# Kernel optimization log

Hardware: AMD Instinct MI355X
Metric: run time of the kernel (lower is better)

## Reference

```python
import jax, jax.numpy as jnp
import numpy as np
from jax import lax

N_QUANTIZE = 256
N_AUX = 28
N_RESCH = 512
N_SKIPCH = 256
KS = 2
DILATIONS = [2 ** i for i in range(10)] * 3  # 30 layers
L = len(DILATIONS)


def _causal_conv(x, w, b, d):
    # x: (B, Cin, T), w: (Cout, Cin, KS) torch Conv1d layout, left-pad => causal
    pad = (w.shape[-1] - 1) * d
    y = lax.conv_general_dilated(x, w, window_strides=(1,), padding=[(pad, 0)],
                                 rhs_dilation=(d,),
                                 dimension_numbers=('NCH', 'OIH', 'NCH'))
    return y + b[None, :, None]


def _conv1x1(x, w, b):
    # x: (B, Cin, T), w: (Cout, Cin)
    return jnp.einsum('oi,bit->bot', w, x) + b[None, :, None]


def setup_inputs() -> dict:
    key = jax.random.key(0)
    ks = jax.random.split(key, 20)
    B, T = 2, 8000
    s = 0.05
    rn = lambda k, shape: (jax.random.normal(k, shape, jnp.float32) * s)
    inp = {
        'x': jax.random.randint(ks[0], (B, T), 0, N_QUANTIZE),
        'h': jax.random.normal(ks[1], (B, N_AUX, T), jnp.float32),
        'causal_w': rn(ks[2], (N_RESCH, N_QUANTIZE, KS)),
        'causal_b': rn(ks[3], (N_RESCH,)),
        'dil_sig_w': rn(ks[4], (L, N_RESCH, N_RESCH, KS)),
        'dil_sig_b': rn(ks[5], (L, N_RESCH)),
        'dil_tanh_w': rn(ks[6], (L, N_RESCH, N_RESCH, KS)),
        'dil_tanh_b': rn(ks[7], (L, N_RESCH)),
        'aux_sig_w': rn(ks[8], (L, N_RESCH, N_AUX)),
        'aux_sig_b': rn(ks[9], (L, N_RESCH)),
        'aux_tanh_w': rn(ks[10], (L, N_RESCH, N_AUX)),
        'aux_tanh_b': rn(ks[11], (L, N_RESCH)),
        'skip_w': rn(ks[12], (L, N_SKIPCH, N_RESCH)),
        'skip_b': rn(ks[13], (L, N_SKIPCH)),
        'res_w': rn(ks[14], (L, N_RESCH, N_RESCH)),
        'res_b': rn(ks[15], (L, N_RESCH)),
        'post1_w': rn(ks[16], (N_SKIPCH, N_SKIPCH)),
        'post1_b': rn(ks[17], (N_SKIPCH,)),
        'post2_w': rn(ks[18], (N_QUANTIZE, N_SKIPCH)),
        'post2_b': rn(ks[19], (N_QUANTIZE,)),
    }
    return inp


def reference(x, h, causal_w, causal_b, dil_sig_w, dil_sig_b, dil_tanh_w, dil_tanh_b,
              aux_sig_w, aux_sig_b, aux_tanh_w, aux_tanh_b, skip_w, skip_b,
              res_w, res_b, post1_w, post1_b, post2_w, post2_b):
    B, T = x.shape
    # _preprocess: onehot (B,T,Q) -> (B,Q,T), then causal conv
    oh = jax.nn.one_hot(x % N_QUANTIZE, N_QUANTIZE, dtype=jnp.float32).transpose(0, 2, 1)
    out = _causal_conv(oh, causal_w, causal_b, 1)  # (B, n_resch, T)
    skip_sum = jnp.zeros((B, N_SKIPCH, T), jnp.float32)
    for l, d in enumerate(DILATIONS):
        sig = _causal_conv(out, dil_sig_w[l], dil_sig_b[l], d) + _conv1x1(h, aux_sig_w[l], aux_sig_b[l])
        tan = _causal_conv(out, dil_tanh_w[l], dil_tanh_b[l], d) + _conv1x1(h, aux_tanh_w[l], aux_tanh_b[l])
        z = jax.nn.sigmoid(sig) * jnp.tanh(tan)
        skip_sum = skip_sum + _conv1x1(z, skip_w[l], skip_b[l])
        out = _conv1x1(z, res_w[l], res_b[l]) + out
    # _postprocess: relu -> 1x1 -> relu -> 1x1 -> (B, T, n_quantize)
    y = jax.nn.relu(skip_sum)
    y = jax.nn.relu(_conv1x1(y, post1_w, post1_b))
    y = _conv1x1(y, post2_w, post2_b)
    return y.transpose(0, 2, 1)
```

## Files before the change

### kernel.cpp

```cpp
#include <hip/hip_runtime.h>
#include <math.h>

#define T_LEN 8000
#define BATCH 2
#define CCH 512
#define SKP 256
#define AUXP 32
#define NQ 256
#define NLAYER 30
#define PADF 512
#define TPAD 8192
#define ROWS (PADF + TPAD)
#define HROWS TPAD

typedef unsigned short hfu;
typedef unsigned int u32;
typedef __attribute__((ext_vector_type(8))) _Float16 half8;
typedef __attribute__((ext_vector_type(4))) float f32x4;

#define GLOAD16(g, l)                                                          \
  __builtin_amdgcn_global_load_lds(                                            \
      (const __attribute__((address_space(1))) void*)(g),                      \
      (__attribute__((address_space(3))) void*)(l), 16, 0, 0)

__device__ inline hfu hfbits(float f) {
  union { _Float16 h; hfu u; } x;
  x.h = (_Float16)f;
  return x.u;
}
__device__ inline u32 pk2(float a, float b) {
  return (u32)hfbits(a) | ((u32)hfbits(b) << 16);
}
__device__ inline uint4 pk8(const float f[8]) {
  return make_uint4(pk2(f[0], f[1]), pk2(f[2], f[3]), pk2(f[4], f[5]), pk2(f[6], f[7]));
}
__device__ inline int ldsL(int row, int ck) {
  return ((row >> 1) << 3) + ((((ck) ^ ((row >> 1) & 3)) << 1) | (row & 1));
}

__global__ __launch_bounds__(256) void zero16(uint4* p, int n) {
  for (int i = blockIdx.x * 256 + threadIdx.x; i < n; i += gridDim.x * 256)
    p[i] = make_uint4(0u, 0u, 0u, 0u);
}

__global__ __launch_bounds__(256) void cvt_dil2b(const float* __restrict__ inS,
                                                 const float* __restrict__ inT,
                                                 hfu* __restrict__ outS, hfu* __restrict__ outT) {
  const long NG = (long)NLAYER * CCH * (CCH / 8);
  for (long g2 = (long)blockIdx.x * 256 + threadIdx.x; g2 < 2 * NG; g2 += (long)gridDim.x * 256) {
    const int sel = (int)(g2 >= NG);
    const long g = sel ? (g2 - NG) : g2;
    const float* in = sel ? inT : inS;
    hfu* out = sel ? outT : outS;
    const int i8 = (int)(g & 63) * 8;
    const int o = (int)((g >> 6) & 511);
    const int l = (int)(g >> 15);
    const float* pp = in + (((size_t)l * CCH + o) * CCH + i8) * 2;
    float4 a = *(const float4*)pp;
    float4 bq = *(const float4*)(pp + 4);
    float4 c = *(const float4*)(pp + 8);
    float4 e = *(const float4*)(pp + 12);
    const float t0[8] = {a.x, a.z, bq.x, bq.z, c.x, c.z, e.x, e.z};
    const float t1[8] = {a.y, a.w, bq.y, bq.w, c.y, c.w, e.y, e.w};
    hfu* ob = out + ((size_t)l * 2 * CCH + o) * CCH + i8;
    *(uint4*)ob = pk8(t0);
    *(uint4*)(ob + (size_t)CCH * CCH) = pk8(t1);
  }
}

__global__ __launch_bounds__(256) void cvt_skipres(const float* __restrict__ skw,
                                                   const float* __restrict__ rsw,
                                                   hfu* __restrict__ out) {
  const long NG = (long)NLAYER * 768 * (CCH / 4);
  for (long g = (long)blockIdx.x * 256 + threadIdx.x; g < NG; g += (long)gridDim.x * 256) {
    const int i4 = (int)(g & 127) * 4;
    const int r = (int)((g >> 7) % 768);
    const int l = (int)(g / (128 * 768));
    const float* src = (r < SKP) ? (skw + ((size_t)l * SKP + r) * CCH + i4)
                                 : (rsw + ((size_t)l * CCH + (r - SKP)) * CCH + i4);
    float4 f = *(const float4*)src;
    *(uint2*)(out + ((size_t)l * 768 + r) * CCH + i4) = make_uint2(pk2(f.x, f.y), pk2(f.z, f.w));
  }
}

__global__ __launch_bounds__(256) void cvt_aux(const float* __restrict__ in, hfu* __restrict__ out) {
  const int N = NLAYER * CCH * AUXP;
  for (int i = blockIdx.x * 256 + threadIdx.x; i < N; i += gridDim.x * 256) {
    const int j = i & 31;
    const int o = (i >> 5) & 511;
    const int l = i >> 14;
    float v = (j < 28) ? in[((size_t)l * CCH + o) * 28 + j] : 0.f;
    out[i] = hfbits(v);
  }
}

__global__ __launch_bounds__(256) void cvt_copy(const float* __restrict__ in, hfu* __restrict__ out, int n) {
  for (int i = blockIdx.x * 256 + threadIdx.x; i < n; i += gridDim.x * 256)
    out[i] = hfbits(in[i]);
}

__global__ __launch_bounds__(256) void cvt_cwt(const float* __restrict__ cw, float* __restrict__ out) {
  const int N = 2 * NQ * CCH;
  for (int i = blockIdx.x * 256 + threadIdx.x; i < N; i += gridDim.x * 256) {
    const int tap = i >> 17;
    const int r = i & 131071;
    const int xq = r >> 9;
    const int o = r & 511;
    out[i] = cw[((size_t)o * NQ + xq) * 2 + tap];
  }
}

__global__ __launch_bounds__(256) void htrans_kernel(const float* __restrict__ h, hfu* __restrict__ hbf) {
  const int b = blockIdx.y;
  const int t = blockIdx.x * 64 + (threadIdx.x & 63);
  const int j0 = threadIdx.x >> 6;
#pragma unroll
  for (int j = j0; j < AUXP; j += 4) {
    float v = (j < 28 && t < T_LEN) ? h[((size_t)b * 28 + j) * T_LEN + t] : 0.f;
    hbf[((size_t)b * HROWS + t) * AUXP + j] = hfbits(v);
  }
}

template <int PRE>
__global__ __launch_bounds__(256) void embed_kernel(const int* __restrict__ x,
                                                    const float* __restrict__ cwt,
                                                    const float* __restrict__ cb,
                                                    float* __restrict__ outf,
                                                    hfu* __restrict__ outb) {
  const int b = blockIdx.y;
  const int t = blockIdx.x * 4 + (threadIdx.x >> 6);
  const int o = (threadIdx.x & 63) * 8;
  const int xc = x[(size_t)b * T_LEN + t] & 255;
  const int xp = (t > 0) ? (x[(size_t)b * T_LEN + t - 1] & 255) : 0;
  const float won = (t > 0) ? 1.f : 0.f;
  const float* c1 = cwt + 131072 + (size_t)xc * CCH + o;
  const float* c0 = cwt + (size_t)xp * CCH + o;
  float v[8];
#pragma unroll
  for (int j = 0; j < 8; ++j) v[j] = cb[o + j] + c1[j] + won * c0[j];
  if (PRE) {
    *(uint4*)&outb[((size_t)b * ROWS + PADF + t) * CCH + o] = pk8(v);
  } else {
    float* po = outf + ((size_t)b * ROWS + PADF + t) * CCH + o;
    *(float4*)po = make_float4(v[0], v[1], v[2], v[3]);
    *(float4*)(po + 4) = make_float4(v[4], v[5], v[6], v[7]);
  }
}

template <int PRE>
__global__ __launch_bounds__(512, 2) void gate_kernel(
    const hfu* __restrict__ actb, const float* __restrict__ actf,
    const hfu* __restrict__ hbf,
    const void* __restrict__ wsp, const void* __restrict__ wtp,
    const hfu* __restrict__ auxs, const hfu* __restrict__ auxt,
    const float* __restrict__ bs1, const float* __restrict__ bs2,
    const float* __restrict__ bt1, const float* __restrict__ bt2,
    hfu* __restrict__ z, int d) {
  extern __shared__ uint4 smd[];
  const int tid = threadIdx.x;
  const int lane = tid & 63, wid = tid >> 6;
  const int wm = wid >> 2, wn = wid & 3;
  const int lr = lane & 15, lq = lane >> 4;

  const int n = blockIdx.x;
  const int f = (n & 7) * 32 + (n >> 3);
  const int tt = f >> 3, inner = f & 7;
  const int o0 = (inner >> 1) * 128;
  const int b = inner & 1;
  const int t0 = tt * 256;

  const int row = 2 * (tid >> 3) + (tid & 1);
  const int ck = ((tid & 7) >> 1) ^ ((tid >> 3) & 3);

  f32x4 accS[4][4] = {};
  f32x4 accT[4][4] = {};

  if (PRE) {
    const hfu* wsPtr = (const hfu*)wsp + ((size_t)CCH + o0 + row) * CCH + ck * 8;
    const hfu* wtPtr = (const hfu*)wtp + ((size_t)CCH + o0 + row) * CCH + ck * 8;
    const hfu* bP0 = actb + ((size_t)b * ROWS + PADF + t0 + row) * CCH + ck * 8;
    const hfu* bP1 = bP0 + (size_t)128 * CCH;
    int offA[4], offB[4];
#pragma unroll
    for (int mr = 0; mr < 4; ++mr) offA[mr] = ldsL(wm * 64 + mr * 16 + lr, lq);
#pragma unroll
    for (int nr = 0; nr < 4; ++nr) offB[nr] = ldsL(wn * 64 + nr * 16 + lr, lq);

    auto stage = [&](int ihs) {
      uint4* dst = smd + (ihs % 3) * 2048;
      if (ihs < 32) {
        GLOAD16(wsPtr, &dst[tid]);
        GLOAD16(wtPtr, &dst[512 + tid]);
        GLOAD16(bP0, &dst[1024 + tid]);
        GLOAD16(bP1, &dst[1536 + tid]);
        if (ihs == 15) {
          wsPtr -= (size_t)CCH * CCH + 480;
          wtPtr -= (size_t)CCH * CCH + 480;
          bP0 -= 480 + (size_t)d * CCH;
          bP1 -= 480 + (size_t)d * CCH;
        } else {
          wsPtr += 32; wtPtr += 32; bP0 += 32; bP1 += 32;
        }
      } else {
        GLOAD16(auxs + (size_t)(o0 + row) * AUXP + ck * 8, &dst[tid]);
        GLOAD16(auxt + (size_t)(o0 + row) * AUXP + ck * 8, &dst[512 + tid]);
        GLOAD16(hbf + ((size_t)b * HROWS + t0 + row) * AUXP + ck * 8, &dst[1024 + tid]);
        GLOAD16(hbf + ((size_t)b * HROWS + t0 + 128 + row) * AUXP + ck * 8, &dst[1536 + tid]);
      }
    };

    stage(0); stage(1); stage(2);
    for (int ih = 0; ih < 33; ++ih) {
      if (ih <= 30)
        asm volatile("s_waitcnt vmcnt(8)" ::: "memory");
      else if (ih == 31)
        asm volatile("s_waitcnt vmcnt(4)" ::: "memory");
      else
        asm volatile("s_waitcnt vmcnt(0)" ::: "memory");
      __builtin_amdgcn_s_barrier();
      __builtin_amdgcn_sched_barrier(0);
      const uint4* base = smd + (ih % 3) * 2048;
      half8 af[4], ag[4], bv[4];
#pragma unroll
      for (int mr = 0; mr < 4; ++mr) {
        af[mr] = *(const half8*)&base[offA[mr]];
        ag[mr] = *(const half8*)&base[512 + offA[mr]];
      }
#pragma unroll
      for (int nr = 0; nr < 4; ++nr) bv[nr] = *(const half8*)&base[1024 + offB[nr]];
      __builtin_amdgcn_s_setprio(1);
#pragma unroll
      for (int mr = 0; mr < 4; ++mr)
#pragma unroll
        for (int nr = 0; nr < 4; ++nr) {
          accS[mr][nr] = __builtin_amdgcn_mfma_f32_16x16x32_f16(af[mr], bv[nr], accS[mr][nr], 0, 0, 0);
          accT[mr][nr] = __builtin_amdgcn_mfma_f32_16x16x32_f16(ag[mr], bv[nr], accT[mr][nr], 0, 0, 0);
        }
      __builtin_amdgcn_s_setprio(0);
      __builtin_amdgcn_sched_barrier(0);
      __builtin_amdgcn_s_barrier();
      if (ih <= 29) stage(ih + 3);
    }
  } else {
    for (int ih = 0; ih < 33; ++ih) {
      uint4* dst = smd + (ih % 3) * 2048;
      if (ih < 32) {
        const int tau = (ih < 16) ? 1 : 0;
        const int koff = (ih & 15) * 32;
        const float* wsf = (const float*)wsp;
        const float* wtf = (const float*)wtp;
        const size_t fb = ((size_t)(o0 + row) * CCH + koff + ck * 8) * 2;
        float vs[8], vt[8];
#pragma unroll
        for (int j = 0; j < 4; ++j) {
          float4 fs = *(const float4*)&wsf[fb + j * 4];
          float4 ft = *(const float4*)&wtf[fb + j * 4];
          vs[2 * j] = tau ? fs.y : fs.x;
          vs[2 * j + 1] = tau ? fs.w : fs.z;
          vt[2 * j] = tau ? ft.y : ft.x;
          vt[2 * j + 1] = tau ? ft.w : ft.z;
        }
        dst[tid] = pk8(vs);
        dst[512 + tid] = pk8(vt);
#pragma unroll
        for (int c = 0; c < 2; ++c) {
          const int rr = row + c * 128;
          const float* ar = actf + ((size_t)b * ROWS + PADF + t0 + rr - (tau ? 0 : d)) * CCH + koff + ck * 8;
          float4 f0 = *(const float4*)&ar[0];
          float4 f1 = *(const float4*)&ar[4];
          float vb[8] = {f0.x, f0.y, f0.z, f0.w, f1.x, f1.y, f1.z, f1.w};
          dst[1024 + c * 512 + tid] = pk8(vb);
        }
      } else {
        dst[tid] = *(const uint4*)&auxs[(size_t)(o0 + row) * AUXP + ck * 8];
        dst[512 + tid] = *(const uint4*)&auxt[(size_t)(o0 + row) * AUXP + ck * 8];
        dst[1024 + tid] = *(const uint4*)&hbf[((size_t)b * HROWS + t0 + row) * AUXP + ck * 8];
        dst[1536 + tid] = *(const uint4*)&hbf[((size_t)b * HROWS + t0 + 128 + row) * AUXP + ck * 8];
      }
      __syncthreads();
      const uint4* base = smd + (ih % 3) * 2048;
      half8 af[4], ag[4], bv[4];
#pragma unroll
      for (int mr = 0; mr < 4; ++mr) {
        const int idx = ldsL(wm * 64 + mr * 16 + lr, lq);
        af[mr] = *(const half8*)&base[idx];
        ag[mr] = *(const half8*)&base[512 + idx];
      }
#pragma unroll
      for (int nr = 0; nr < 4; ++nr)
        bv[nr] = *(const half8*)&base[1024 + ldsL(wn * 64 + nr * 16 + lr, lq)];
#pragma unroll
      for (int mr = 0; mr < 4; ++mr)
#pragma unroll
        for (int nr = 0; nr < 4; ++nr) {
          accS[mr][nr] = __builtin_amdgcn_mfma_f32_16x16x32_f16(af[mr], bv[nr], accS[mr][nr], 0, 0, 0);
          accT[mr][nr] = __builtin_amdgcn_mfma_f32_16x16x32_f16(ag[mr], bv[nr], accT[mr][nr], 0, 0, 0);
        }
      __syncthreads();
    }
  }

#pragma unroll
  for (int mr = 0; mr < 4; ++mr) {
    const int ob = o0 + wm * 64 + mr * 16 + lq * 4;
    float4 x1 = *(const float4*)&bs1[ob];
    float4 x2 = *(const float4*)&bs2[ob];
    float4 y1 = *(const float4*)&bt1[ob];
    float4 y2 = *(const float4*)&bt2[ob];
    const float sb[4] = {x1.x + x2.x, x1.y + x2.y, x1.z + x2.z, x1.w + x2.w};
    const float tb[4] = {y1.x + y2.x, y1.y + y2.y, y1.z + y2.z, y1.w + y2.w};
#pragma unroll
    for (int nr = 0; nr < 4; ++nr) {
      const int t = t0 + wn * 64 + nr * 16 + lr;
      float zv[4];
#pragma unroll
      for (int j = 0; j < 4; ++j) {
        float sv = accS[mr][nr][j] + sb[j];
        float tv = accT[mr][nr][j] + tb[j];
        float sg = __builtin_amdgcn_rcpf(1.f + __expf(-sv));
        float e2 = __expf(2.f * tv);
        float th = 1.f - 2.f * __builtin_amdgcn_rcpf(e2 + 1.f);
        zv[j] = sg * th;
      }
      *(uint2*)&z[((size_t)b * HROWS + t) * CCH + ob] = make_uint2(pk2(zv[0], zv[1]), pk2(zv[2], zv[3]));
    }
  }
}

template <int PRE>
__global__ __launch_bounds__(512, 4) void update_kernel(
    const hfu* __restrict__ z, const void* __restrict__ wp,
    const float* __restrict__ skwf, const float* __restrict__ rswf,
    const float* __restrict__ skb, const float* __restrict__ rsb,
    float* __restrict__ skip, hfu* __restrict__ skiph,
    float* __restrict__ outf, hfu* __restrict__ outb) {
  __shared__ uint4 sm[3072];
  const int tid = threadIdx.x;
  const int lane = tid & 63, wid = tid >> 6;
  const int wm = wid >> 1, wn = wid & 1;
  const int lr = lane & 15, lq = lane >> 4;

  const int n = blockIdx.x;
  const int xcd = n & 7, j = n >> 3;
  const int ttl = j / 12, inner = j % 12;
  const int tt = xcd * 8 + ttl;
  if (tt > 62) return;
  const int rg = inner >> 1, b = inner & 1;
  const int r0 = rg * 128;
  const int t0 = tt * 128;

  f32x4 acc[2][4] = {};
  const int row = 2 * (tid >> 3) + (tid & 1);
  const int ck = ((tid & 7) >> 1) ^ ((tid >> 3) & 3);

  if (PRE) {
    const hfu* wPtr = (const hfu*)wp + (size_t)(r0 + row) * CCH + ck * 8;
    const hfu* zPtr = z + ((size_t)b * HROWS + t0 + row) * CCH + ck * 8;
    int offa[2], offb[4];
#pragma unroll
    for (int mr = 0; mr < 2; ++mr) offa[mr] = ldsL(wm * 32 + mr * 16 + lr, lq);
#pragma unroll
    for (int nr = 0; nr < 4; ++nr) offb[nr] = ldsL(wn * 64 + nr * 16 + lr, lq);

    auto stage_u = [&](int ihs) {
      uint4* dst = sm + (ihs % 3) * 1024;
      GLOAD16(wPtr, &dst[tid]);
      GLOAD16(zPtr, &dst[512 + tid]);
      wPtr += 32; zPtr += 32;
    };
    stage_u(0); stage_u(1); stage_u(2);
    for (int ih = 0; ih < 16; ++ih) {
      if (ih <= 13)
        asm volatile("s_waitcnt vmcnt(4)" ::: "memory");
      else if (ih == 14)
        asm volatile("s_waitcnt vmcnt(2)" ::: "memory");
      else
        asm volatile("s_waitcnt vmcnt(0)" ::: "memory");
      __builtin_amdgcn_s_barrier();
      __builtin_amdgcn_sched_barrier(0);
      const uint4* base = sm + (ih % 3) * 1024;
      half8 av[2], bv[4];
#pragma unroll
      for (int mr = 0; mr < 2; ++mr) av[mr] = *(const half8*)&base[offa[mr]];
#pragma unroll
      for (int nr = 0; nr < 4; ++nr) bv[nr] = *(const half8*)&base[512 + offb[nr]];
      __builtin_amdgcn_s_setprio(1);
#pragma unroll
      for (int mr = 0; mr < 2; ++mr)
#pragma unroll
        for (int nr = 0; nr < 4; ++nr)
          acc[mr][nr] = __builtin_amdgcn_mfma_f32_16x16x32_f16(av[mr], bv[nr], acc[mr][nr], 0, 0, 0);
      __builtin_amdgcn_s_setprio(0);
      __builtin_amdgcn_sched_barrier(0);
      __builtin_amdgcn_s_barrier();
      if (ih <= 12) stage_u(ih + 3);
    }
  } else {
    for (int ih = 0; ih < 16; ++ih) {
      uint4* dst = sm + (ih % 3) * 1024;
      const int k0 = ih * 32;
      const int R = r0 + row;
      const float* src = (R < SKP) ? (skwf + (size_t)R * CCH + k0 + ck * 8)
                                   : (rswf + (size_t)(R - SKP) * CCH + k0 + ck * 8);
      float4 f0 = *(const float4*)&src[0];
      float4 f1 = *(const float4*)&src[4];
      float v[8] = {f0.x, f0.y, f0.z, f0.w, f1.x, f1.y, f1.z, f1.w};
      dst[tid] = pk8(v);
      dst[512 + tid] = *(const uint4*)&z[((size_t)b * HROWS + t0 + row) * CCH + k0 + ck * 8];
      __syncthreads();
      const uint4* base = sm + (ih % 3) * 1024;
      half8 av[2], bv[4];
#pragma unroll
      for (int mr = 0; mr < 2; ++mr) av[mr] = *(const half8*)&base[ldsL(wm * 32 + mr * 16 + lr, lq)];
#pragma unroll
      for (int nr = 0; nr < 4; ++nr) bv[nr] = *(const half8*)&base[512 + ldsL(wn * 64 + nr * 16 + lr, lq)];
#pragma unroll
      for (int mr = 0; mr < 2; ++mr)
#pragma unroll
        for (int nr = 0; nr < 4; ++nr)
          acc[mr][nr] = __builtin_amdgcn_mfma_f32_16x16x32_f16(av[mr], bv[nr], acc[mr][nr], 0, 0, 0);
      __syncthreads();
    }
  }

  const bool iskip = (r0 < SKP);
#pragma unroll
  for (int mr = 0; mr < 2; ++mr) {
    const int R = r0 + wm * 32 + mr * 16 + lq * 4;
#pragma unroll
    for (int nr = 0; nr < 4; ++nr) {
      const int t = t0 + wn * 64 + nr * 16 + lr;
      if (t < T_LEN) {
        if (iskip) {
          float4 bb = *(const float4*)&skb[R];
          if (PRE) {
            hfu* ps = &skiph[((size_t)b * T_LEN + t) * SKP + R];
            uint2 old = *(uint2*)ps;
            const _Float16* hp = (const _Float16*)&old;
            float v0 = (float)hp[0] + acc[mr][nr][0] + bb.x;
            float v1 = (float)hp[1] + acc[mr][nr][1] + bb.y;
            float v2 = (float)hp[2] + acc[mr][nr][2] + bb.z;
            float v3 = (float)hp[3] + acc[mr][nr][3] + bb.w;
            *(uint2*)ps = make_uint2(pk2(v0, v1), pk2(v2, v3));
          } else {
            float4* p = (float4*)&skip[((size_t)b * T_LEN + t) * SKP + R];
            float4 v = *p;
            v.x += acc[mr][nr][0] + bb.x;
            v.y += acc[mr][nr][1] + bb.y;
            v.z += acc[mr][nr][2] + bb.z;
            v.w += acc[mr][nr][3] + bb.w;
            *p = v;
          }
        } else {
          const int rr = R - SKP;
          float4 bb = *(const float4*)&rsb[rr];
          if (PRE) {
            hfu* pb = &outb[((size_t)b * ROWS + PADF + t) * CCH + rr];
            uint2 old = *(uint2*)pb;
            const _Float16* hp = (const _Float16*)&old;
            float v0 = (float)hp[0] + acc[mr][nr][0] + bb.x;
            float v1 = (float)hp[1] + acc[mr][nr][1] + bb.y;
            float v2 = (float)hp[2] + acc[mr][nr][2] + bb.z;
            float v3 = (float)hp[3] + acc[mr][nr][3] + bb.w;
            *(uint2*)pb = make_uint2(pk2(v0, v1), pk2(v2, v3));
          } else {
            float4* p = (float4*)&outf[((size_t)b * ROWS + PADF + t) * CCH + rr];
            float4 v = *p;
            v.x += acc[mr][nr][0] + bb.x;
            v.y += acc[mr][nr][1] + bb.y;
            v.z += acc[mr][nr][2] + bb.z;
            v.w += acc[mr][nr][3] + bb.w;
            *p = v;
          }
        }
      }
    }
  }
}

template <int PRE>
__global__ __launch_bounds__(256, 2) void post1_kernel(const float* __restrict__ skip,
                                                       const hfu* __restrict__ skiph,
                                                       const hfu* __restrict__ w,
                                                       const float* __restrict__ bias,
                                                       hfu* __restrict__ y1) {
  __shared__ uint4 sm[2048];
  uint4* sA = sm;
  uint4* sB = sm + 1024;
  const int tid = threadIdx.x;
  const int lane = tid & 63, wid = tid >> 6;
  const int wm = wid >> 1, wn = wid & 1;
  const int lr = lane & 15, lq = lane >> 4;
  const int t0 = blockIdx.x * 128;
  const int r0 = blockIdx.y * 128;
  const int b = blockIdx.z;
  f32x4 acc[4][4] = {};
  for (int kt = 0; kt < 4; ++kt) {
#pragma unroll
    for (int c = 0; c < 4; ++c) {
      const int cb = c * 256 + wid * 64;
      const int ch = cb + lane;
      const int ksub = ch >> 7, mn = ch & 127;
      const int k0 = kt * 64 + ksub * 8;
      GLOAD16(w + (size_t)(r0 + mn) * SKP + k0, &sA[cb]);
      int row = t0 + mn;
      if (row > T_LEN - 1) row = T_LEN - 1;
      if (PRE) {
        uint4 u = *(const uint4*)&skiph[((size_t)b * T_LEN + row) * SKP + k0];
        const _Float16* hp = (const _Float16*)&u;
        float v[8];
#pragma unroll
        for (int jj = 0; jj < 8; ++jj) v[jj] = fmaxf((float)hp[jj], 0.f);
        sB[ch] = pk8(v);
      } else {
        const float* src = skip + ((size_t)b * T_LEN + row) * SKP + k0;
        float4 f0 = *(const float4*)&src[0];
        float4 f1 = *(const float4*)&src[4];
        float v[8] = {fmaxf(f0.x, 0.f), fmaxf(f0.y, 0.f), fmaxf(f0.z, 0.f), fmaxf(f0.w, 0.f),
                      fmaxf(f1.x, 0.f), fmaxf(f1.y, 0.f), fmaxf(f1.z, 0.f), fmaxf(f1.w, 0.f)};
        sB[ch] = pk8(v);
      }
    }
    __syncthreads();
#pragma unroll
    for (int ks = 0; ks < 2; ++ks) {
      const int kb = (ks * 4 + lq) * 128;
      half8 av[4], bv[4];
#pragma unroll
      for (int r = 0; r < 4; ++r) {
        av[r] = *(const half8*)&sA[kb + wm * 64 + r * 16 + lr];
        bv[r] = *(const half8*)&sB[kb + wn * 64 + r * 16 + lr];
      }
#pragma unroll
      for (int mr = 0; mr < 4; ++mr)
#pragma unroll
        for (int nr = 0; nr < 4; ++nr)
          acc[mr][nr] = __builtin_amdgcn_mfma_f32_16x16x32_f16(av[mr], bv[nr], acc[mr][nr], 0, 0, 0);
    }
    __syncthreads();
  }
#pragma unroll
  for (int mr = 0; mr < 4; ++mr) {
    const int ob = r0 + wm * 64 + mr * 16 + lq * 4;
    float4 bb = *(const float4*)&bias[ob];
    const float bs[4] = {bb.x, bb.y, bb.z, bb.w};
#pragma unroll
    for (int nr = 0; nr < 4; ++nr) {
      const int t = t0 + wn * 64 + nr * 16 + lr;
      float v[4];
#pragma unroll
      for (int jj = 0; jj < 4; ++jj) v[jj] = fmaxf(acc[mr][nr][jj] + bs[jj], 0.f);
      *(uint2*)&y1[((size_t)b * HROWS + t) * SKP + ob] = make_uint2(pk2(v[0], v[1]), pk2(v[2], v[3]));
    }
  }
}

__global__ __launch_bounds__(256, 2) void post2_kernel(const hfu* __restrict__ y1,
                                                       const hfu* __restrict__ w,
                                                       const float* __restrict__ bias,
                                                       float* __restrict__ outp) {
  __shared__ uint4 sm[2048];
  uint4* sA = sm;
  uint4* sB = sm + 1024;
  const int tid = threadIdx.x;
  const int lane = tid & 63, wid = tid >> 6;
  const int wm = wid >> 1, wn = wid & 1;
  const int lr = lane & 15, lq = lane >> 4;
  const int t0 = blockIdx.x * 128;
  const int r0 = blockIdx.y * 128;
  const int b = blockIdx.z;
  f32x4 acc[4][4] = {};
  for (int kt = 0; kt < 4; ++kt) {
#pragma unroll
    for (int c = 0; c < 4; ++c) {
      const int cb = c * 256 + wid * 64;
      const int ch = cb + lane;
      const int ksub = ch >> 7, mn = ch & 127;
      const int k0 = kt * 64 + ksub * 8;
      GLOAD16(w + (size_t)(r0 + mn) * SKP + k0, &sA[cb]);
      GLOAD16(y1 + ((size_t)b * HROWS + t0 + mn) * SKP + k0, &sB[cb]);
    }
    __syncthreads();
#pragma unroll
    for (int ks = 0; ks < 2; ++ks) {
      const int kb = (ks * 4 + lq) * 128;
      half8 av[4], bv[4];
#pragma unroll
      for (int r = 0; r < 4; ++r) {
        av[r] = *(const half8*)&sA[kb + wm * 64 + r * 16 + lr];
        bv[r] = *(const half8*)&sB[kb + wn * 64 + r * 16 + lr];
      }
#pragma unroll
      for (int mr = 0; mr < 4; ++mr)
#pragma unroll
        for (int nr = 0; nr < 4; ++nr)
          acc[mr][nr] = __builtin_amdgcn_mfma_f32_16x16x32_f16(av[mr], bv[nr], acc[mr][nr], 0, 0, 0);
    }
    __syncthreads();
  }
#pragma unroll
  for (int mr = 0; mr < 4; ++mr) {
    const int ob = r0 + wm * 64 + mr * 16 + lq * 4;
    float4 bb = *(const float4*)&bias[ob];
#pragma unroll
    for (int nr = 0; nr < 4; ++nr) {
      const int t = t0 + wn * 64 + nr * 16 + lr;
      if (t < T_LEN) {
        float4 v;
        v.x = acc[mr][nr][0] + bb.x;
        v.y = acc[mr][nr][1] + bb.y;
        v.z = acc[mr][nr][2] + bb.z;
        v.w = acc[mr][nr][3] + bb.w;
        *(float4*)&outp[((size_t)b * T_LEN + t) * NQ + ob] = v;
      }
    }
  }
}

extern "C" void kernel_launch(void* const* d_in, const int* in_sizes, int n_in,
                              void* d_out, int out_size, void* d_ws, size_t ws_size,
                              hipStream_t stream) {
  const int* x = (const int*)d_in[0];
  const float* h = (const float*)d_in[1];
  const float* causal_w = (const float*)d_in[2];
  const float* causal_b = (const float*)d_in[3];
  const float* dil_sig_w = (const float*)d_in[4];
  const float* dil_sig_b = (const float*)d_in[5];
  const float* dil_tanh_w = (const float*)d_in[6];
  const float* dil_tanh_b = (const float*)d_in[7];
  const float* aux_sig_w = (const float*)d_in[8];
  const float* aux_sig_b = (const float*)d_in[9];
  const float* aux_tanh_w = (const float*)d_in[10];
  const float* aux_tanh_b = (const float*)d_in[11];
  const float* skip_w = (const float*)d_in[12];
  const float* skip_b = (const float*)d_in[13];
  const float* res_w = (const float*)d_in[14];
  const float* res_b = (const float*)d_in[15];
  const float* post1_w = (const float*)d_in[16];
  const float* post1_b = (const float*)d_in[17];
  const float* post2_w = (const float*)d_in[18];
  const float* post2_b = (const float*)d_in[19];
  float* outp = (float*)d_out;

  hipFuncSetAttribute((const void*)gate_kernel<1>,
                      hipFuncAttributeMaxDynamicSharedMemorySize, 98304);
  hipFuncSetAttribute((const void*)gate_kernel<0>,
                      hipFuncAttributeMaxDynamicSharedMemorySize, 98304);

  char* p = (char*)d_ws;
  auto alloc = [&](size_t bytes) {
    char* r = p;
    p += (bytes + 255) & ~(size_t)255;
    return r;
  };
  float* outf = (float*)alloc((size_t)BATCH * ROWS * CCH * 4);
  float* skip = (float*)alloc((size_t)BATCH * T_LEN * SKP * 4);
  hfu* zb = (hfu*)alloc((size_t)BATCH * HROWS * CCH * 2);
  hfu* hbf = (hfu*)alloc((size_t)BATCH * HROWS * AUXP * 2);
  hfu* auxsb = (hfu*)alloc((size_t)NLAYER * CCH * AUXP * 2);
  hfu* auxtb = (hfu*)alloc((size_t)NLAYER * CCH * AUXP * 2);
  hfu* p1b = (hfu*)alloc((size_t)NQ * SKP * 2);
  hfu* p2b = (hfu*)alloc((size_t)NQ * SKP * 2);
  float* cwt = (float*)alloc((size_t)2 * NQ * CCH * 4);
  hfu* skiph = (hfu*)alloc((size_t)BATCH * T_LEN * SKP * 2);
  hfu* y1 = zb;
  hfu* outb = (hfu*)alloc((size_t)BATCH * ROWS * CCH * 2);
  hfu* dilS = (hfu*)alloc((size_t)NLAYER * 2 * CCH * CCH * 2);
  hfu* dilT = (hfu*)alloc((size_t)NLAYER * 2 * CCH * CCH * 2);
  hfu* wsr = (hfu*)alloc((size_t)NLAYER * 768 * CCH * 2);
  const bool pre = ((size_t)(p - (char*)d_ws) <= ws_size);

  cvt_aux<<<256, 256, 0, stream>>>(aux_sig_w, auxsb);
  cvt_aux<<<256, 256, 0, stream>>>(aux_tanh_w, auxtb);
  cvt_copy<<<64, 256, 0, stream>>>(post1_w, p1b, NQ * SKP);
  cvt_copy<<<64, 256, 0, stream>>>(post2_w, p2b, NQ * SKP);
  cvt_cwt<<<1024, 256, 0, stream>>>(causal_w, cwt);
  if (pre) {
    cvt_dil2b<<<2048, 256, 0, stream>>>(dil_sig_w, dil_tanh_w, dilS, dilT);
    cvt_skipres<<<2048, 256, 0, stream>>>(skip_w, res_w, wsr);
  }

  if (pre) {
    zero16<<<512, 256, 0, stream>>>((uint4*)skiph, (int)((size_t)BATCH * T_LEN * SKP * 2 / 16));
    for (int b = 0; b < BATCH; ++b) {
      zero16<<<32, 256, 0, stream>>>((uint4*)(outb + (size_t)b * ROWS * CCH), PADF * CCH * 2 / 16);
      zero16<<<48, 256, 0, stream>>>((uint4*)(outb + ((size_t)b * ROWS + PADF + T_LEN) * CCH),
                                     (TPAD - T_LEN) * CCH * 2 / 16);
    }
  } else {
    zero16<<<512, 256, 0, stream>>>((uint4*)skip, (int)((size_t)BATCH * T_LEN * SKP * 4 / 16));
    for (int b = 0; b < BATCH; ++b) {
      zero16<<<64, 256, 0, stream>>>((uint4*)(outf + (size_t)b * ROWS * CCH), PADF * CCH * 4 / 16);
      zero16<<<96, 256, 0, stream>>>((uint4*)(outf + ((size_t)b * ROWS + PADF + T_LEN) * CCH),
                                     (TPAD - T_LEN) * CCH * 4 / 16);
    }
  }

  htrans_kernel<<<dim3(128, 2), 256, 0, stream>>>(h, hbf);
  if (pre)
    embed_kernel<1><<<dim3(2000, 2), 256, 0, stream>>>(x, cwt, causal_b, nullptr, outb);
  else
    embed_kernel<0><<<dim3(2000, 2), 256, 0, stream>>>(x, cwt, causal_b, outf, nullptr);

  for (int l = 0; l < NLAYER; ++l) {
    const int d = 1 << (l % 10);
    if (pre) {
      gate_kernel<1><<<256, 512, 98304, stream>>>(
          outb, nullptr, hbf, dilS + (size_t)l * 2 * CCH * CCH, dilT + (size_t)l * 2 * CCH * CCH,
          auxsb + (size_t)l * CCH * AUXP, auxtb + (size_t)l * CCH * AUXP,
          dil_sig_b + (size_t)l * CCH, aux_sig_b + (size_t)l * CCH,
          dil_tanh_b + (size_t)l * CCH, aux_tanh_b + (size_t)l * CCH, zb, d);
      update_kernel<1><<<768, 512, 0, stream>>>(
          zb, wsr + (size_t)l * 768 * CCH, nullptr, nullptr,
          skip_b + (size_t)l * SKP, res_b + (size_t)l * CCH, nullptr, skiph, nullptr, outb);
    } else {
      gate_kernel<0><<<256, 512, 98304, stream>>>(
          nullptr, outf, hbf, dil_sig_w + (size_t)l * CCH * CCH * 2,
          dil_tanh_w + (size_t)l * CCH * CCH * 2,
          auxsb + (size_t)l * CCH * AUXP, auxtb + (size_t)l * CCH * AUXP,
          dil_sig_b + (size_t)l * CCH, aux_sig_b + (size_t)l * CCH,
          dil_tanh_b + (size_t)l * CCH, aux_tanh_b + (size_t)l * CCH, zb, d);
      update_kernel<0><<<768, 512, 0, stream>>>(
          zb, nullptr, skip_w + (size_t)l * SKP * CCH, res_w + (size_t)l * CCH * CCH,
          skip_b + (size_t)l * SKP, res_b + (size_t)l * CCH, skip, nullptr, outf, nullptr);
    }
  }

  if (pre)
    post1_kernel<1><<<dim3(63, 2, BATCH), 256, 0, stream>>>(nullptr, skiph, p1b, post1_b, y1);
  else
    post1_kernel<0><<<dim3(63, 2, BATCH), 256, 0, stream>>>(skip, nullptr, p1b, post1_b, y1);
  post2_kernel<<<dim3(63, 2, BATCH), 256, 0, stream>>>(y1, p2b, post2_b, outp);
}
```

Measured before the change: 2.165 ms.

## Load activation operand directly into registers and double-buffer weight tiles in LDS

The gate kernel stops staging the activation (B) operand through LDS and loads each lane's MFMA fragments straight from global memory into registers, keeping only the weight tiles in a two-slot LDS buffer. This cuts LDS from 96 KB dynamic to 32 KB static. The update kernel's three-stage async pipeline is also reduced to double buffering with one barrier per step. This removes LDS traffic and pressure, but exposes global-load latency with vmcnt(0) waits every iteration and shortens the prefetch depth.

```diff
diff --git a/kernel.cpp b/kernel.cpp
--- a/kernel.cpp
+++ b/kernel.cpp
@@ -33,6 +33,12 @@
 }
 __device__ inline uint4 pk8(const float f[8]) {
   return make_uint4(pk2(f[0], f[1]), pk2(f[2], f[3]), pk2(f[4], f[5]), pk2(f[6], f[7]));
+}
+__device__ inline half8 cvt8(const float f[8]) {
+  half8 r;
+#pragma unroll
+  for (int j = 0; j < 8; ++j) r[j] = (_Float16)f[j];
+  return r;
 }
 __device__ inline int ldsL(int row, int ck) {
   return ((row >> 1) << 3) + ((((ck) ^ ((row >> 1) & 3)) << 1) | (row & 1));
@@ -156,7 +162,7 @@
     const float* __restrict__ bs1, const float* __restrict__ bs2,
     const float* __restrict__ bt1, const float* __restrict__ bt2,
     hfu* __restrict__ z, int d) {
-  extern __shared__ uint4 smd[];
+  __shared__ uint4 smA[2048];
   const int tid = threadIdx.x;
   const int lane = tid & 63, wid = tid >> 6;
   const int wm = wid >> 2, wn = wid & 3;
@@ -175,59 +181,68 @@
   f32x4 accS[4][4] = {};
   f32x4 accT[4][4] = {};
 
+  int offA[4];
+#pragma unroll
+  for (int mr = 0; mr < 4; ++mr) offA[mr] = ldsL(wm * 64 + mr * 16 + lr, lq);
+  int brow[4];
+#pragma unroll
+  for (int nr = 0; nr < 4; ++nr) brow[nr] = t0 + wn * 64 + nr * 16 + lr;
+
   if (PRE) {
     const hfu* wsPtr = (const hfu*)wsp + ((size_t)CCH + o0 + row) * CCH + ck * 8;
     const hfu* wtPtr = (const hfu*)wtp + ((size_t)CCH + o0 + row) * CCH + ck * 8;
-    const hfu* bP0 = actb + ((size_t)b * ROWS + PADF + t0 + row) * CCH + ck * 8;
-    const hfu* bP1 = bP0 + (size_t)128 * CCH;
-    int offA[4], offB[4];
-#pragma unroll
-    for (int mr = 0; mr < 4; ++mr) offA[mr] = ldsL(wm * 64 + mr * 16 + lr, lq);
-#pragma unroll
-    for (int nr = 0; nr < 4; ++nr) offB[nr] = ldsL(wn * 64 + nr * 16 + lr, lq);
-
-    auto stage = [&](int ihs) {
-      uint4* dst = smd + (ihs % 3) * 2048;
+    const hfu* bP[4];
+#pragma unroll
+    for (int nr = 0; nr < 4; ++nr)
+      bP[nr] = actb + ((size_t)b * ROWS + PADF + brow[nr]) * CCH + lq * 8;
+
+    auto stageA = [&](int ihs) {
+      uint4* dst = smA + (ihs & 1) * 1024;
       if (ihs < 32) {
         GLOAD16(wsPtr, &dst[tid]);
         GLOAD16(wtPtr, &dst[512 + tid]);
-        GLOAD16(bP0, &dst[1024 + tid]);
-        GLOAD16(bP1, &dst[1536 + tid]);
         if (ihs == 15) {
           wsPtr -= (size_t)CCH * CCH + 480;
           wtPtr -= (size_t)CCH * CCH + 480;
-          bP0 -= 480 + (size_t)d * CCH;
-          bP1 -= 480 + (size_t)d * CCH;
         } else {
-          wsPtr += 32; wtPtr += 32; bP0 += 32; bP1 += 32;
+          wsPtr += 32;
+          wtPtr += 32;
         }
       } else {
         GLOAD16(auxs + (size_t)(o0 + row) * AUXP + ck * 8, &dst[tid]);
         GLOAD16(auxt + (size_t)(o0 + row) * AUXP + ck * 8, &dst[512 + tid]);
-        GLOAD16(hbf + ((size_t)b * HROWS + t0 + row) * AUXP + ck * 8, &dst[1024 + tid]);
-        GLOAD16(hbf + ((size_t)b * HROWS + t0 + 128 + row) * AUXP + ck * 8, &dst[1536 + tid]);
       }
     };
 
-    stage(0); stage(1); stage(2);
+    stageA(0);
     for (int ih = 0; ih < 33; ++ih) {
-      if (ih <= 30)
-        asm volatile("s_waitcnt vmcnt(8)" ::: "memory");
-      else if (ih == 31)
-        asm volatile("s_waitcnt vmcnt(4)" ::: "memory");
-      else
-        asm volatile("s_waitcnt vmcnt(0)" ::: "memory");
+      asm volatile("s_waitcnt vmcnt(0)" ::: "memory");
       __builtin_amdgcn_s_barrier();
       __builtin_amdgcn_sched_barrier(0);
-      const uint4* base = smd + (ih % 3) * 2048;
-      half8 af[4], ag[4], bv[4];
+      half8 bv[4];
+      if (ih < 32) {
+#pragma unroll
+        for (int nr = 0; nr < 4; ++nr) bv[nr] = *(const half8*)bP[nr];
+        if (ih == 15) {
+#pragma unroll
+          for (int nr = 0; nr < 4; ++nr) bP[nr] -= 480 + (size_t)d * CCH;
+        } else {
+#pragma unroll
+          for (int nr = 0; nr < 4; ++nr) bP[nr] += 32;
+        }
+      } else {
+#pragma unroll
+        for (int nr = 0; nr < 4; ++nr)
+          bv[nr] = *(const half8*)&hbf[((size_t)b * HROWS + brow[nr]) * AUXP + lq * 8];
+      }
+      if (ih < 32) stageA(ih + 1);
+      const uint4* base = smA + (ih & 1) * 1024;
+      half8 af[4], ag[4];
 #pragma unroll
       for (int mr = 0; mr < 4; ++mr) {
         af[mr] = *(const half8*)&base[offA[mr]];
         ag[mr] = *(const half8*)&base[512 + offA[mr]];
       }
-#pragma unroll
-      for (int nr = 0; nr < 4; ++nr) bv[nr] = *(const half8*)&base[1024 + offB[nr]];
       __builtin_amdgcn_s_setprio(1);
 #pragma unroll
       for (int mr = 0; mr < 4; ++mr)
@@ -238,12 +253,10 @@
         }
       __builtin_amdgcn_s_setprio(0);
       __builtin_amdgcn_sched_barrier(0);
-      __builtin_amdgcn_s_barrier();
-      if (ih <= 29) stage(ih + 3);
     }
   } else {
     for (int ih = 0; ih < 33; ++ih) {
-      uint4* dst = smd + (ih % 3) * 2048;
+      uint4* dst = smA + (ih & 1) * 1024;
       if (ih < 32) {
         const int tau = (ih < 16) ? 1 : 0;
         const int koff = (ih & 15) * 32;
@@ -262,33 +275,33 @@
         }
         dst[tid] = pk8(vs);
         dst[512 + tid] = pk8(vt);
-#pragma unroll
-        for (int c = 0; c < 2; ++c) {
-          const int rr = row + c * 128;
-          const float* ar = actf + ((size_t)b * ROWS + PADF + t0 + rr - (tau ? 0 : d)) * CCH + koff + ck * 8;
-          float4 f0 = *(const float4*)&ar[0];
-          float4 f1 = *(const float4*)&ar[4];
-          float vb[8] = {f0.x, f0.y, f0.z, f0.w, f1.x, f1.y, f1.z, f1.w};
-          dst[1024 + c * 512 + tid] = pk8(vb);
-        }
       } else {
         dst[tid] = *(const uint4*)&auxs[(size_t)(o0 + row) * AUXP + ck * 8];
         dst[512 + tid] = *(const uint4*)&auxt[(size_t)(o0 + row) * AUXP + ck * 8];
-        dst[1024 + tid] = *(const uint4*)&hbf[((size_t)b * HROWS + t0 + row) * AUXP + ck * 8];
-        dst[1536 + tid] = *(const uint4*)&hbf[((size_t)b * HROWS + t0 + 128 + row) * AUXP + ck * 8];
       }
       __syncthreads();
-      const uint4* base = smd + (ih % 3) * 2048;
-      half8 af[4], ag[4], bv[4];
+      half8 bv[4];
+      if (ih < 32) {
+        const int tau = (ih < 16) ? 1 : 0;
+        const int koff = (ih & 15) * 32;
+#pragma unroll
+        for (int nr = 0; nr < 4; ++nr) {
+          const float* ar = actf + ((size_t)b * ROWS + PADF + brow[nr] - (tau ? 0 : d)) * CCH + koff + lq * 8;
+          float v[8] = {ar[0], ar[1], ar[2], ar[3], ar[4], ar[5], ar[6], ar[7]};
+          bv[nr] = cvt8(v);
+        }
+      } else {
+#pragma unroll
+        for (int nr = 0; nr < 4; ++nr)
+          bv[nr] = *(const half8*)&hbf[((size_t)b * HROWS + brow[nr]) * AUXP + lq * 8];
+      }
+      const uint4* base = smA + (ih & 1) * 1024;
+      half8 af[4], ag[4];
 #pragma unroll
       for (int mr = 0; mr < 4; ++mr) {
-        const int idx = ldsL(wm * 64 + mr * 16 + lr, lq);
-        af[mr] = *(const half8*)&base[idx];
-        ag[mr] = *(const half8*)&base[512 + idx];
-      }
-#pragma unroll
-      for (int nr = 0; nr < 4; ++nr)
-        bv[nr] = *(const half8*)&base[1024 + ldsL(wn * 64 + nr * 16 + lr, lq)];
+        af[mr] = *(const half8*)&base[offA[mr]];
+        ag[mr] = *(const half8*)&base[512 + offA[mr]];
+      }
 #pragma unroll
       for (int mr = 0; mr < 4; ++mr)
 #pragma unroll
@@ -334,7 +347,7 @@
     const float* __restrict__ skb, const float* __restrict__ rsb,
     float* __restrict__ skip, hfu* __restrict__ skiph,
     float* __restrict__ outf, hfu* __restrict__ outb) {
-  __shared__ uint4 sm[3072];
+  __shared__ uint4 sm[2048];
   const int tid = threadIdx.x;
   const int lane = tid & 63, wid = tid >> 6;
   const int wm = wid >> 1, wn = wid & 1;
@@ -362,28 +375,25 @@
 #pragma unroll
     for (int nr = 0; nr < 4; ++nr) offb[nr] = ldsL(wn * 64 + nr * 16 + lr, lq);
 
-    auto stage_u = [&](int ihs) {
-      uint4* dst = sm + (ihs % 3) * 1024;
-      GLOAD16(wPtr, &dst[tid]);
-      GLOAD16(zPtr, &dst[512 + tid]);
-      wPtr += 32; zPtr += 32;
-    };
-    stage_u(0); stage_u(1); stage_u(2);
+    GLOAD16(wPtr, &sm[tid]);
+    GLOAD16(zPtr, &sm[512 + tid]);
+    wPtr += 32; zPtr += 32;
     for (int ih = 0; ih < 16; ++ih) {
-      if (ih <= 13)
-        asm volatile("s_waitcnt vmcnt(4)" ::: "memory");
-      else if (ih == 14)
-        asm volatile("s_waitcnt vmcnt(2)" ::: "memory");
-      else
-        asm volatile("s_waitcnt vmcnt(0)" ::: "memory");
+      asm volatile("s_waitcnt vmcnt(0)" ::: "memory");
       __builtin_amdgcn_s_barrier();
       __builtin_amdgcn_sched_barrier(0);
-      const uint4* base = sm + (ih % 3) * 1024;
+      const uint4* base = sm + ((ih & 1) << 10);
       half8 av[2], bv[4];
 #pragma unroll
       for (int mr = 0; mr < 2; ++mr) av[mr] = *(const half8*)&base[offa[mr]];
 #pragma unroll
       for (int nr = 0; nr < 4; ++nr) bv[nr] = *(const half8*)&base[512 + offb[nr]];
+      if (ih < 15) {
+        uint4* dst = sm + (((ih + 1) & 1) << 10);
+        GLOAD16(wPtr, &dst[tid]);
+        GLOAD16(zPtr, &dst[512 + tid]);
+        wPtr += 32; zPtr += 32;
+      }
       __builtin_amdgcn_s_setprio(1);
 #pragma unroll
       for (int mr = 0; mr < 2; ++mr)
@@ -392,12 +402,10 @@
           acc[mr][nr] = __builtin_amdgcn_mfma_f32_16x16x32_f16(av[mr], bv[nr], acc[mr][nr], 0, 0, 0);
       __builtin_amdgcn_s_setprio(0);
       __builtin_amdgcn_sched_barrier(0);
-      __builtin_amdgcn_s_barrier();
-      if (ih <= 12) stage_u(ih + 3);
     }
   } else {
     for (int ih = 0; ih < 16; ++ih) {
-      uint4* dst = sm + (ih % 3) * 1024;
+      const int base = (ih & 1) * 1024;
       const int k0 = ih * 32;
       const int R = r0 + row;
       const float* src = (R < SKP) ? (skwf + (size_t)R * CCH + k0 + ck * 8)
@@ -405,15 +413,14 @@
       float4 f0 = *(const float4*)&src[0];
       float4 f1 = *(const float4*)&src[4];
       float v[8] = {f0.x, f0.y, f0.z, f0.w, f1.x, f1.y, f1.z, f1.w};
-      dst[tid] = pk8(v);
-      dst[512 + tid] = *(const uint4*)&z[((size_t)b * HROWS + t0 + row) * CCH + k0 + ck * 8];
+      sm[base + tid] = pk8(v);
+      sm[base + 512 + tid] = *(const uint4*)&z[((size_t)b * HROWS + t0 + row) * CCH + k0 + ck * 8];
       __syncthreads();
-      const uint4* base = sm + (ih % 3) * 1024;
       half8 av[2], bv[4];
 #pragma unroll
-      for (int mr = 0; mr < 2; ++mr) av[mr] = *(const half8*)&base[ldsL(wm * 32 + mr * 16 + lr, lq)];
-#pragma unroll
-      for (int nr = 0; nr < 4; ++nr) bv[nr] = *(const half8*)&base[512 + ldsL(wn * 64 + nr * 16 + lr, lq)];
+      for (int mr = 0; mr < 2; ++mr) av[mr] = *(const half8*)&sm[base + ldsL(wm * 32 + mr * 16 + lr, lq)];
+#pragma unroll
+      for (int nr = 0; nr < 4; ++nr) bv[nr] = *(const half8*)&sm[base + 512 + ldsL(wn * 64 + nr * 16 + lr, lq)];
 #pragma unroll
       for (int mr = 0; mr < 2; ++mr)
 #pragma unroll
@@ -642,11 +649,6 @@
   const float* post2_b = (const float*)d_in[19];
   float* outp = (float*)d_out;
 
-  hipFuncSetAttribute((const void*)gate_kernel<1>,
-                      hipFuncAttributeMaxDynamicSharedMemorySize, 98304);
-  hipFuncSetAttribute((const void*)gate_kernel<0>,
-                      hipFuncAttributeMaxDynamicSharedMemorySize, 98304);
-
   char* p = (char*)d_ws;
   auto alloc = [&](size_t bytes) {
     char* r = p;
@@ -705,7 +707,7 @@
   for (int l = 0; l < NLAYER; ++l) {
     const int d = 1 << (l % 10);
     if (pre) {
-      gate_kernel<1><<<256, 512, 98304, stream>>>(
+      gate_kernel<1><<<256, 512, 0, stream>>>(
           outb, nullptr, hbf, dilS + (size_t)l * 2 * CCH * CCH, dilT + (size_t)l * 2 * CCH * CCH,
           auxsb + (size_t)l * CCH * AUXP, auxtb + (size_t)l * CCH * AUXP,
           dil_sig_b + (size_t)l * CCH, aux_sig_b + (size_t)l * CCH,
@@ -714,7 +716,7 @@
           zb, wsr + (size_t)l * 768 * CCH, nullptr, nullptr,
           skip_b + (size_t)l * SKP, res_b + (size_t)l * CCH, nullptr, skiph, nullptr, outb);
     } else {
-      gate_kernel<0><<<256, 512, 98304, stream>>>(
+      gate_kernel<0><<<256, 512, 0, stream>>>(
           nullptr, outf, hbf, dil_sig_w + (size_t)l * CCH * CCH * 2,
           dil_tanh_w + (size_t)l * CCH * CCH * 2,
           auxsb + (size_t)l * CCH * AUXP, auxtb + (size_t)l * CCH * AUXP,
```

Result: slower. 2.647 ms (+22.3%).
